# Performance work log

Measured on AMD Instinct MI355X. Metric: run time of the kernel, lower is better.

The kernel has to match this reference:

```python
import jax, jax.numpy as jnp
import numpy as np

EMB_DIM = 1024
N_HEADS = 16
HEAD_DIM = EMB_DIM // N_HEADS
WINDOW = 128
B, T = 4, 2048


def setup_inputs() -> dict:
    key = jax.random.key(0)
    k1, k2, k3 = jax.random.split(key, 3)
    x = jax.random.normal(k1, (B, T, EMB_DIM), dtype=jnp.float32)
    # nn.Linear weights: stored as [out, in], applied as x @ W^T
    s1 = 1.0 / np.sqrt(EMB_DIM)
    w_qkv = jax.random.uniform(k2, (3 * EMB_DIM, EMB_DIM), jnp.float32, -s1, s1)
    w_out = jax.random.uniform(k3, (EMB_DIM, EMB_DIM), jnp.float32, -s1, s1)
    return {"x": x, "w_qkv": w_qkv, "w_out": w_out}


def reference(x, w_qkv, w_out):
    Bs, Ts, C = x.shape
    scale = HEAD_DIM ** -0.5
    qkv = x @ w_qkv.T                                   # [B,T,3C]
    qkv = qkv.reshape(Bs, Ts, 3, N_HEADS, HEAD_DIM)
    qkv = jnp.transpose(qkv, (2, 0, 3, 1, 4))           # [3,B,H,T,D]
    q, k, v = qkv[0], qkv[1], qkv[2]
    scores = jnp.einsum('bhtd,bhsd->bhts', q, k) * scale  # [B,H,T,T]
    i = jnp.arange(Ts)[:, None]
    j = jnp.arange(Ts)[None, :]
    # causal AND within sliding window: i - WINDOW <= j <= i
    allowed = (j <= i) & (j >= i - WINDOW)               # [T,T] bool
    scores = jnp.where(allowed[None, None], scores, -jnp.inf)
    attn = jax.nn.softmax(scores, axis=-1)
    out = jnp.einsum('bhts,bhsd->bhtd', attn, v)         # [B,H,T,D]
    out = jnp.transpose(out, (0, 2, 1, 3)).reshape(Bs, Ts, C)
    return out @ w_out.T
```

## Files before the change

kernel.cpp:

```cpp
#include <hip/hip_runtime.h>
#include <hip/hip_bf16.h>
#include <stdint.h>

typedef __attribute__((ext_vector_type(8))) short bf16x8;
typedef __attribute__((ext_vector_type(4))) float f32x4;
typedef __attribute__((ext_vector_type(4))) unsigned short u16x4;

#define B_ 4
#define T_ 2048
#define C_ 1024
#define H_ 16
#define D_ 64

__device__ __forceinline__ unsigned short f2bf(float f) {
  union { float f; uint32_t u; } v; v.f = f;
  uint32_t u = v.u;
  uint32_t r = (u + 0x7FFFu + ((u >> 16) & 1u)) >> 16;
  return (unsigned short)r;
}

__global__ void __launch_bounds__(256) cast_f32_bf16(const float* __restrict__ src,
                                                     unsigned short* __restrict__ dst,
                                                     int n4) {
  int i = blockIdx.x * 256 + threadIdx.x;
  if (i >= n4) return;
  float4 f = ((const float4*)src)[i];
  u16x4 o;
  o[0] = f2bf(f.x); o[1] = f2bf(f.y); o[2] = f2bf(f.z); o[3] = f2bf(f.w);
  ((u16x4*)dst)[i] = o;
}

template <int MODE>
__global__ void __launch_bounds__(256) gemm_bt(const unsigned short* __restrict__ A,
                                               const unsigned short* __restrict__ Bm,
                                               unsigned short* __restrict__ qb,
                                               unsigned short* __restrict__ kb,
                                               unsigned short* __restrict__ vb,
                                               float* __restrict__ fo) {
  __shared__ short lds[16896];
  const int tid = threadIdx.x;
  const int bm = blockIdx.y * 128;
  const int bn = blockIdx.x * 128;

  const int wave = tid >> 6;
  const int l = tid & 63;
  const int wm = wave >> 1, wn = wave & 1;
  const int lm = l & 15, lq = l >> 4;
  const int lr = l >> 2;
  const int lc = (l & 3) << 3;

  f32x4 acc[4][4];
#pragma unroll
  for (int i = 0; i < 4; i++)
#pragma unroll
    for (int j = 0; j < 4; j++) acc[i][j] = (f32x4){0.f, 0.f, 0.f, 0.f};

  const unsigned short* gsrc[4];
  int ldoff[4];
#pragma unroll
  for (int i = 0; i < 4; i++) {
    int c = wave * 4 + i;
    if (c < 8) {
      gsrc[i] = A + (size_t)(bm + 16 * c + lr) * 1024 + lc;
      ldoff[i] = (16 * c) * 32;
    } else {
      gsrc[i] = Bm + (size_t)(bn + 16 * (c - 8) + lr) * 1024 + lc;
      ldoff[i] = 8192 + (16 * (c - 8)) * 32;
    }
  }

#define STAGE(curb, kk)                                                          \
  do {                                                                           \
    _Pragma("unroll")                                                            \
    for (int i = 0; i < 4; i++) {                                                \
      __builtin_amdgcn_global_load_lds(                                          \
          (__attribute__((address_space(1))) void*)(uintptr_t)(const void*)(gsrc[i] + (kk)), \
          (__attribute__((address_space(3))) void*)(lds + ldoff[i] + (curb) * 4096),         \
          16, 0, 0);                                                             \
    }                                                                            \
  } while (0)

  STAGE(0, 0);
  int cur = 0;
  __syncthreads();

  for (int k0 = 0; k0 < 1024; k0 += 32) {
    if (k0 + 32 < 1024) STAGE(cur ^ 1, k0 + 32);
    bf16x8 af[4], bfr[4];
#pragma unroll
    for (int i = 0; i < 4; i++)
      af[i] = *(const bf16x8*)&lds[cur * 4096 + (wm * 64 + 16 * i + lm) * 32 + 8 * lq];
#pragma unroll
    for (int j = 0; j < 4; j++)
      bfr[j] = *(const bf16x8*)&lds[8192 + cur * 4096 + (wn * 64 + 16 * j + lm) * 32 + 8 * lq];
#pragma unroll
    for (int i = 0; i < 4; i++)
#pragma unroll
      for (int j = 0; j < 4; j++)
        acc[i][j] = __builtin_amdgcn_mfma_f32_16x16x32_bf16(af[i], bfr[j], acc[i][j], 0, 0, 0);
    __syncthreads();
    cur ^= 1;
  }
#undef STAGE

  if (MODE == 0) {
    if (bn >= 2048) {
#pragma unroll
      for (int i = 0; i < 4; i++)
#pragma unroll
        for (int j = 0; j < 4; j++) {
          int m0 = bm + wm * 64 + 16 * i + 4 * lq;
          int n = (bn - 2048) + wn * 64 + 16 * j + lm;
          int h = n >> 6, d = n & 63;
          int b = m0 >> 11, t = m0 & 2047;
          u16x4 o;
#pragma unroll
          for (int r = 0; r < 4; r++) o[r] = f2bf(acc[i][j][r]);
          *(u16x4*)&vb[(((size_t)(b * 16 + h)) * 64 + d) * 2048 + t] = o;
        }
    } else {
#pragma unroll
      for (int i = 0; i < 4; i++)
#pragma unroll
        for (int j = 0; j < 4; j++)
#pragma unroll
          for (int r = 0; r < 4; r++)
            lds[(wm * 64 + 16 * i + 4 * lq + r) * 132 + wn * 64 + 16 * j + lm] =
                (short)f2bf(acc[i][j][r]);
      __syncthreads();
#pragma unroll
      for (int k = 0; k < 8; k++) {
        int c = tid + 256 * k;
        int row = c >> 4;
        int col = (c & 15) << 3;
        bf16x8 v = *(const bf16x8*)&lds[row * 132 + col];
        int m = bm + row, n = bn + col;
        int which = n >> 10, rem = n & 1023;
        int h = rem >> 6, d = rem & 63;
        int b = m >> 11, t = m & 2047;
        unsigned short* dst = (which == 0) ? qb : kb;
        *(bf16x8*)&dst[(((size_t)(b * 16 + h)) * 2048 + t) * 64 + d] = v;
      }
    }
  } else {
#pragma unroll
    for (int i = 0; i < 4; i++)
#pragma unroll
      for (int j = 0; j < 4; j++)
#pragma unroll
        for (int r = 0; r < 4; r++) {
          int m = bm + wm * 64 + 16 * i + 4 * lq + r;
          int n = bn + wn * 64 + 16 * j + lm;
          fo[(size_t)m * 1024 + n] = acc[i][j][r];
        }
  }
}

__global__ void __launch_bounds__(256) attn_swa(const unsigned short* __restrict__ Qb,
                                               const unsigned short* __restrict__ Kb,
                                               const unsigned short* __restrict__ Vt,
                                               unsigned short* __restrict__ Ob) {
  __shared__ short P[4][16 * 40];
  const int wv = threadIdx.x >> 6;
  const int l = threadIdx.x & 63;
  const int wid = blockIdx.x * 4 + wv;
  const int bh = wid >> 7;
  const int t0 = (wid & 127) << 4;
  const int lm = l & 15, lq = l >> 4;
  const size_t base = (size_t)bh * (T_ * D_);

  bf16x8 aq0 = *(const bf16x8*)(Qb + base + (size_t)(t0 + lm) * 64 + 8 * lq);
  bf16x8 aq1 = *(const bf16x8*)(Qb + base + (size_t)(t0 + lm) * 64 + 32 + 8 * lq);

  float mst[4], lst[4];
  f32x4 Oa[4];
#pragma unroll
  for (int r = 0; r < 4; r++) { mst[r] = -1e30f; lst[r] = 0.f; }
#pragma unroll
  for (int jt = 0; jt < 4; jt++) Oa[jt] = (f32x4){0.f, 0.f, 0.f, 0.f};

  const float cs = 0.125f * 1.44269504f;
  int jstart = t0 - 128; if (jstart < 0) jstart = 0;

  for (int j0 = jstart; j0 < t0 + 16; j0 += 32) {
    f32x4 S[2];
#pragma unroll
    for (int hh = 0; hh < 2; hh++) {
      int kr = j0 + 16 * hh + lm; if (kr > T_ - 1) kr = T_ - 1;
      bf16x8 bk0 = *(const bf16x8*)(Kb + base + (size_t)kr * 64 + 8 * lq);
      bf16x8 bk1 = *(const bf16x8*)(Kb + base + (size_t)kr * 64 + 32 + 8 * lq);
      f32x4 s = (f32x4){0.f, 0.f, 0.f, 0.f};
      s = __builtin_amdgcn_mfma_f32_16x16x32_bf16(aq0, bk0, s, 0, 0, 0);
      s = __builtin_amdgcn_mfma_f32_16x16x32_bf16(aq1, bk1, s, 0, 0, 0);
      S[hh] = s;
    }
    float p0s[4], p1s[4], al[4];
#pragma unroll
    for (int r = 0; r < 4; r++) {
      int t = t0 + 4 * lq + r;
      int ja = j0 + lm, jb = j0 + 16 + lm;
      float s0 = ((ja <= t) && (ja + 128 >= t)) ? S[0][r] * cs : -1e30f;
      float s1 = ((jb <= t) && (jb + 128 >= t)) ? S[1][r] * cs : -1e30f;
      float m2 = fmaxf(s0, s1);
#pragma unroll
      for (int off = 1; off < 16; off <<= 1) m2 = fmaxf(m2, __shfl_xor(m2, off));
      float mn = fmaxf(mst[r], m2);
      float a = __builtin_amdgcn_exp2f(mst[r] - mn);
      float p0 = __builtin_amdgcn_exp2f(s0 - mn);
      float p1 = __builtin_amdgcn_exp2f(s1 - mn);
      float ps = p0 + p1;
#pragma unroll
      for (int off = 1; off < 16; off <<= 1) ps += __shfl_xor(ps, off);
      lst[r] = lst[r] * a + ps;
      mst[r] = mn;
      al[r] = a; p0s[r] = p0; p1s[r] = p1;
    }
#pragma unroll
    for (int jt = 0; jt < 4; jt++)
#pragma unroll
      for (int r = 0; r < 4; r++) Oa[jt][r] *= al[r];
#pragma unroll
    for (int r = 0; r < 4; r++) {
      P[wv][(4 * lq + r) * 40 + lm] = (short)f2bf(p0s[r]);
      P[wv][(4 * lq + r) * 40 + 16 + lm] = (short)f2bf(p1s[r]);
    }
    bf16x8 pa = *(const bf16x8*)&P[wv][lm * 40 + 8 * lq];
#pragma unroll
    for (int jt = 0; jt < 4; jt++) {
      bf16x8 vf = *(const bf16x8*)(Vt + base + (size_t)(16 * jt + lm) * 2048 + j0 + 8 * lq);
      Oa[jt] = __builtin_amdgcn_mfma_f32_16x16x32_bf16(pa, vf, Oa[jt], 0, 0, 0);
    }
  }
  const int b = bh >> 4, h = bh & 15;
#pragma unroll
  for (int r = 0; r < 4; r++) {
    float inv = 1.0f / lst[r];
    int t = t0 + 4 * lq + r;
#pragma unroll
    for (int jt = 0; jt < 4; jt++) {
      int c = h * 64 + 16 * jt + lm;
      Ob[((size_t)(b * T_ + t)) * 1024 + c] = f2bf(Oa[jt][r] * inv);
    }
  }
}

extern "C" void kernel_launch(void* const* d_in, const int* in_sizes, int n_in,
                              void* d_out, int out_size, void* d_ws, size_t ws_size,
                              hipStream_t stream) {
  const float* x = (const float*)d_in[0];
  const float* w_qkv = (const float*)d_in[1];
  const float* w_out = (const float*)d_in[2];
  float* out = (float*)d_out;

  unsigned short* xb = (unsigned short*)d_ws;
  unsigned short* wqkvb = xb + (size_t)8192 * 1024;
  unsigned short* woutb = wqkvb + (size_t)3072 * 1024;
  unsigned short* qb = woutb + (size_t)1024 * 1024;
  unsigned short* kb = qb + (size_t)64 * 2048 * 64;
  unsigned short* vb = kb + (size_t)64 * 2048 * 64;

  cast_f32_bf16<<<8192, 256, 0, stream>>>(x, xb, 8192 * 1024 / 4);
  cast_f32_bf16<<<3072, 256, 0, stream>>>(w_qkv, wqkvb, 3072 * 1024 / 4);
  cast_f32_bf16<<<1024, 256, 0, stream>>>(w_out, woutb, 1024 * 1024 / 4);

  gemm_bt<0><<<dim3(24, 64), 256, 0, stream>>>(xb, wqkvb, qb, kb, vb, nullptr);

  attn_swa<<<2048, 256, 0, stream>>>(qb, kb, vb, xb);

  gemm_bt<1><<<dim3(8, 64), 256, 0, stream>>>(xb, woutb, nullptr, nullptr, nullptr, out);
}
```

Before: 229.7 us.

## Enlarge QKV GEMM tile to 256x128 and merge cast kernels into one launch

The QKV projection GEMM now uses 256x128 block tiles. Each wave computes a 128x64 sub-tile with 32 accumulators, so B fragments are reused across two A halves and global B traffic per output drops. The three fp32-to-bf16 cast launches are merged into a single kernel that picks its source by block index, saving two launches. In exchange the GEMM has higher register pressure (launch_bounds 256,2), fewer blocks (768 vs 1536), and a two-pass LDS epilogue with an extra barrier.

Measured after the change: 229.9 us. About the same (+0.1%).

```diff
diff --git a/kernel.cpp b/kernel.cpp
--- a/kernel.cpp
+++ b/kernel.cpp
@@ -19,29 +19,158 @@
   return (unsigned short)r;
 }
 
-__global__ void __launch_bounds__(256) cast_f32_bf16(const float* __restrict__ src,
-                                                     unsigned short* __restrict__ dst,
-                                                     int n4) {
-  int i = blockIdx.x * 256 + threadIdx.x;
-  if (i >= n4) return;
+__global__ void __launch_bounds__(256) cast_all(const float* __restrict__ x,
+                                                const float* __restrict__ wqkv,
+                                                const float* __restrict__ wout,
+                                                unsigned short* __restrict__ xb,
+                                                unsigned short* __restrict__ wqkvb,
+                                                unsigned short* __restrict__ woutb) {
+  int bid = blockIdx.x;
+  const float* src; unsigned short* dst; int i;
+  if (bid < 8192)       { src = x;    dst = xb;    i = bid * 256 + threadIdx.x; }
+  else if (bid < 11264) { src = wqkv; dst = wqkvb; i = (bid - 8192) * 256 + threadIdx.x; }
+  else                  { src = wout; dst = woutb; i = (bid - 11264) * 256 + threadIdx.x; }
   float4 f = ((const float4*)src)[i];
   u16x4 o;
   o[0] = f2bf(f.x); o[1] = f2bf(f.y); o[2] = f2bf(f.z); o[3] = f2bf(f.w);
   ((u16x4*)dst)[i] = o;
 }
 
-template <int MODE>
-__global__ void __launch_bounds__(256) gemm_bt(const unsigned short* __restrict__ A,
-                                               const unsigned short* __restrict__ Bm,
-                                               unsigned short* __restrict__ qb,
-                                               unsigned short* __restrict__ kb,
-                                               unsigned short* __restrict__ vb,
-                                               float* __restrict__ fo) {
-  __shared__ short lds[16896];
+__global__ void __launch_bounds__(256, 2) gemm_qkv(const unsigned short* __restrict__ A,
+                                                   const unsigned short* __restrict__ Bm,
+                                                   unsigned short* __restrict__ qb,
+                                                   unsigned short* __restrict__ kb,
+                                                   unsigned short* __restrict__ vb) {
+  __shared__ short lds[24576];
+  const int tid = threadIdx.x;
+  const int bm = blockIdx.y * 256;
+  const int bn = blockIdx.x * 128;
+
+  const int wave = tid >> 6;
+  const int l = tid & 63;
+  const int wm = wave >> 1, wn = wave & 1;
+  const int lm = l & 15, lq = l >> 4;
+  const int lr = l >> 2;
+  const int lc = (l & 3) << 3;
+
+  f32x4 acc[8][4];
+#pragma unroll
+  for (int i = 0; i < 8; i++)
+#pragma unroll
+    for (int j = 0; j < 4; j++) acc[i][j] = (f32x4){0.f, 0.f, 0.f, 0.f};
+
+  const unsigned short* gs[6];
+  int ldo[6];
+#pragma unroll
+  for (int i = 0; i < 6; i++) {
+    int c = wave * 6 + i;
+    if (c < 16) {
+      gs[i] = A + (size_t)(bm + 16 * c + lr) * 1024 + lc;
+      ldo[i] = c * 512;
+    } else {
+      gs[i] = Bm + (size_t)(bn + 16 * (c - 16) + lr) * 1024 + lc;
+      ldo[i] = 8192 + (c - 16) * 512;
+    }
+  }
+
+#define STAGE(curb, kk)                                                          \
+  do {                                                                           \
+    _Pragma("unroll")                                                            \
+    for (int i = 0; i < 6; i++) {                                                \
+      __builtin_amdgcn_global_load_lds(                                          \
+          (__attribute__((address_space(1))) void*)(uintptr_t)(const void*)(gs[i] + (kk)), \
+          (__attribute__((address_space(3))) void*)(lds + ldo[i] + (curb) * 12288),        \
+          16, 0, 0);                                                             \
+    }                                                                            \
+  } while (0)
+
+  STAGE(0, 0);
+  int cur = 0;
+  __syncthreads();
+
+  for (int k0 = 0; k0 < 1024; k0 += 32) {
+    if (k0 + 32 < 1024) STAGE(cur ^ 1, k0 + 32);
+    const short* As_ = lds + cur * 12288;
+    const short* Bs_ = lds + cur * 12288 + 8192;
+    bf16x8 Bf[4];
+#pragma unroll
+    for (int j = 0; j < 4; j++)
+      Bf[j] = *(const bf16x8*)&Bs_[(wn * 64 + 16 * j + lm) * 32 + 8 * lq];
+#pragma unroll
+    for (int h = 0; h < 2; h++) {
+      bf16x8 Af[4];
+#pragma unroll
+      for (int i = 0; i < 4; i++)
+        Af[i] = *(const bf16x8*)&As_[(wm * 128 + 64 * h + 16 * i + lm) * 32 + 8 * lq];
+#pragma unroll
+      for (int i = 0; i < 4; i++)
+#pragma unroll
+        for (int j = 0; j < 4; j++)
+          acc[4 * h + i][j] =
+              __builtin_amdgcn_mfma_f32_16x16x32_bf16(Af[i], Bf[j], acc[4 * h + i][j], 0, 0, 0);
+    }
+    __syncthreads();
+    cur ^= 1;
+  }
+#undef STAGE
+
+  if (bn >= 2048) {
+#pragma unroll
+    for (int h = 0; h < 2; h++)
+#pragma unroll
+      for (int i = 0; i < 4; i++)
+#pragma unroll
+        for (int j = 0; j < 4; j++) {
+          int m0 = bm + wm * 128 + 64 * h + 16 * i + 4 * lq;
+          int n = (bn - 2048) + wn * 64 + 16 * j + lm;
+          int hh = n >> 6, d = n & 63;
+          int b = m0 >> 11, t = m0 & 2047;
+          u16x4 o;
+#pragma unroll
+          for (int r = 0; r < 4; r++) o[r] = f2bf(acc[4 * h + i][j][r]);
+          *(u16x4*)&vb[(((size_t)(b * 16 + hh)) * 64 + d) * 2048 + t] = o;
+        }
+  } else {
+#pragma unroll
+    for (int p = 0; p < 2; ++p) {
+      if (p) __syncthreads();
+      if (wm == p) {
+#pragma unroll
+        for (int h = 0; h < 2; h++)
+#pragma unroll
+          for (int i = 0; i < 4; i++)
+#pragma unroll
+            for (int j = 0; j < 4; j++)
+#pragma unroll
+              for (int r = 0; r < 4; r++)
+                lds[(64 * h + 16 * i + 4 * lq + r) * 132 + wn * 64 + 16 * j + lm] =
+                    (short)f2bf(acc[4 * h + i][j][r]);
+      }
+      __syncthreads();
+#pragma unroll
+      for (int k = 0; k < 8; k++) {
+        int c = tid + 256 * k;
+        int row = c >> 4;
+        int col = (c & 15) << 3;
+        bf16x8 v = *(const bf16x8*)&lds[row * 132 + col];
+        int m = bm + 128 * p + row, n = bn + col;
+        int which = n >> 10, rem = n & 1023;
+        int hh = rem >> 6, d = rem & 63;
+        int b = m >> 11, t = m & 2047;
+        unsigned short* dst = (which == 0) ? qb : kb;
+        *(bf16x8*)&dst[(((size_t)(b * 16 + hh)) * 2048 + t) * 64 + d] = v;
+      }
+    }
+  }
+}
+
+__global__ void __launch_bounds__(256) gemm_out(const unsigned short* __restrict__ A,
+                                                const unsigned short* __restrict__ Bm,
+                                                float* __restrict__ fo) {
+  __shared__ short lds[16384];
   const int tid = threadIdx.x;
   const int bm = blockIdx.y * 128;
   const int bn = blockIdx.x * 128;
-
   const int wave = tid >> 6;
   const int l = tid & 63;
   const int wm = wave >> 1, wn = wave & 1;
@@ -103,57 +232,16 @@
   }
 #undef STAGE
 
-  if (MODE == 0) {
-    if (bn >= 2048) {
-#pragma unroll
-      for (int i = 0; i < 4; i++)
-#pragma unroll
-        for (int j = 0; j < 4; j++) {
-          int m0 = bm + wm * 64 + 16 * i + 4 * lq;
-          int n = (bn - 2048) + wn * 64 + 16 * j + lm;
-          int h = n >> 6, d = n & 63;
-          int b = m0 >> 11, t = m0 & 2047;
-          u16x4 o;
-#pragma unroll
-          for (int r = 0; r < 4; r++) o[r] = f2bf(acc[i][j][r]);
-          *(u16x4*)&vb[(((size_t)(b * 16 + h)) * 64 + d) * 2048 + t] = o;
-        }
-    } else {
-#pragma unroll
-      for (int i = 0; i < 4; i++)
-#pragma unroll
-        for (int j = 0; j < 4; j++)
-#pragma unroll
-          for (int r = 0; r < 4; r++)
-            lds[(wm * 64 + 16 * i + 4 * lq + r) * 132 + wn * 64 + 16 * j + lm] =
-                (short)f2bf(acc[i][j][r]);
-      __syncthreads();
-#pragma unroll
-      for (int k = 0; k < 8; k++) {
-        int c = tid + 256 * k;
-        int row = c >> 4;
-        int col = (c & 15) << 3;
-        bf16x8 v = *(const bf16x8*)&lds[row * 132 + col];
-        int m = bm + row, n = bn + col;
-        int which = n >> 10, rem = n & 1023;
-        int h = rem >> 6, d = rem & 63;
-        int b = m >> 11, t = m & 2047;
-        unsigned short* dst = (which == 0) ? qb : kb;
-        *(bf16x8*)&dst[(((size_t)(b * 16 + h)) * 2048 + t) * 64 + d] = v;
+#pragma unroll
+  for (int i = 0; i < 4; i++)
+#pragma unroll
+    for (int j = 0; j < 4; j++)
+#pragma unroll
+      for (int r = 0; r < 4; r++) {
+        int m = bm + wm * 64 + 16 * i + 4 * lq + r;
+        int n = bn + wn * 64 + 16 * j + lm;
+        fo[(size_t)m * 1024 + n] = acc[i][j][r];
       }
-    }
-  } else {
-#pragma unroll
-    for (int i = 0; i < 4; i++)
-#pragma unroll
-      for (int j = 0; j < 4; j++)
-#pragma unroll
-        for (int r = 0; r < 4; r++) {
-          int m = bm + wm * 64 + 16 * i + 4 * lq + r;
-          int n = bn + wn * 64 + 16 * j + lm;
-          fo[(size_t)m * 1024 + n] = acc[i][j][r];
-        }
-  }
 }
 
 __global__ void __launch_bounds__(256) attn_swa(const unsigned short* __restrict__ Qb,
@@ -259,13 +347,11 @@
   unsigned short* kb = qb + (size_t)64 * 2048 * 64;
   unsigned short* vb = kb + (size_t)64 * 2048 * 64;
 
-  cast_f32_bf16<<<8192, 256, 0, stream>>>(x, xb, 8192 * 1024 / 4);
-  cast_f32_bf16<<<3072, 256, 0, stream>>>(w_qkv, wqkvb, 3072 * 1024 / 4);
-  cast_f32_bf16<<<1024, 256, 0, stream>>>(w_out, woutb, 1024 * 1024 / 4);
-
-  gemm_bt<0><<<dim3(24, 64), 256, 0, stream>>>(xb, wqkvb, qb, kb, vb, nullptr);
+  cast_all<<<12288, 256, 0, stream>>>(x, w_qkv, w_out, xb, wqkvb, woutb);
+
+  gemm_qkv<<<dim3(24, 32), 256, 0, stream>>>(xb, wqkvb, qb, kb, vb);
 
   attn_swa<<<2048, 256, 0, stream>>>(qb, kb, vb, xb);
 
-  gemm_bt<1><<<dim3(8, 64), 256, 0, stream>>>(xb, woutb, nullptr, nullptr, nullptr, out);
-}
+  gemm_out<<<dim3(8, 64), 256, 0, stream>>>(xb, woutb, out);
+}
```
